# Performance work log

Measured on AMD Instinct MI355X. Metric: run time of the kernel, lower is better.

Reference implementation:

```python
import jax, jax.numpy as jnp
import numpy as np
import math

B, L, LC = 2, 2048, 2048
D_MODEL, D_CROSS, D_HEAD = 1024, 1024, 64
N_HEADS = D_MODEL // D_HEAD
D6 = D_HEAD // 6  # freq bands per spatial axis (k-diffusion AxialRoPE, 3 axes)
EPS = 1e-6


def rope_freqs():
    n = N_HEADS * D6
    f = jnp.exp(jnp.linspace(math.log(math.pi), math.log(10.0 * math.pi), n + 1)[:-1])
    return f.reshape(D6, N_HEADS).T  # [nh, d6]


def rope_theta(pos):
    # pos: [b, l, 3] -> theta: [b, nh, l, 3*d6]
    f = rope_freqs()
    th = jnp.concatenate([pos[..., None, a:a + 1] * f for a in range(3)], axis=-1)  # [b,l,nh,3*d6]
    return jnp.moveaxis(th, -2, -3)


def apply_rotary(x, theta):
    d = theta.shape[-1]
    x1, x2, x3 = x[..., :d], x[..., d:2 * d], x[..., 2 * d:]
    c, s = jnp.cos(theta), jnp.sin(theta)
    return jnp.concatenate([x1 * c - x2 * s, x2 * c + x1 * s, x3], axis=-1)


def rms_norm(x, scale, eps=EPS):
    ms = jnp.mean(x * x, axis=-1, keepdims=True)
    return x * (scale * jax.lax.rsqrt(ms + eps))


def cosine_scale(q, k, scale, eps=EPS):
    s = jnp.sqrt(scale)[:, None, None]  # [nh,1,1]
    qn = q * (s * jax.lax.rsqrt(jnp.sum(q * q, axis=-1, keepdims=True) + eps))
    kn = k * (s * jax.lax.rsqrt(jnp.sum(k * k, axis=-1, keepdims=True) + eps))
    return qn, kn


def setup_inputs():
    key = jax.random.key(0)
    ks = jax.random.split(key, 8)
    return {
        "x": jax.random.normal(ks[0], (B, L, D_MODEL), jnp.float32),
        "pos": jax.random.uniform(ks[1], (B, L, 3), jnp.float32),
        "x_cross": jax.random.normal(ks[2], (B, LC, D_CROSS), jnp.float32),
        "pos_cross": jax.random.uniform(ks[3], (B, LC, 3), jnp.float32),
        "norm_scale": jnp.ones((D_MODEL,), jnp.float32),
        "norm_cross_scale": jnp.ones((D_CROSS,), jnp.float32),
        "q_w": jax.random.normal(ks[4], (D_MODEL, D_MODEL), jnp.float32) * 0.02,
        "kv_w": jax.random.normal(ks[5], (2 * D_MODEL, D_CROSS), jnp.float32) * 0.02,
        "head_scale": jnp.full((N_HEADS,), 10.0, jnp.float32),
        "out_w": jax.random.normal(ks[6], (D_MODEL, D_MODEL), jnp.float32) * 0.02,
    }


def reference(x, pos, x_cross, pos_cross, norm_scale, norm_cross_scale, q_w, kv_w, head_scale, out_w):
    skip = x
    xn = rms_norm(x, norm_scale)
    xc = rms_norm(x_cross, norm_cross_scale)
    q = xn @ q_w.T                       # [b,l,d]
    kv = xc @ kv_w.T                     # [b,lc,2d]
    b, l, _ = q.shape
    lc = kv.shape[1]
    q = q.reshape(b, l, N_HEADS, D_HEAD).transpose(0, 2, 1, 3)          # [b,nh,l,e]
    kv = kv.reshape(b, lc, 2, N_HEADS, D_HEAD)                          # (t nh e) factorization
    k = kv[:, :, 0].transpose(0, 2, 1, 3)
    v = kv[:, :, 1].transpose(0, 2, 1, 3)
    q, k = cosine_scale(q, k, head_scale)
    q = apply_rotary(q, rope_theta(pos))
    k = apply_rotary(k, rope_theta(pos_cross))
    attn = jax.nn.softmax(jnp.einsum('bhqe,bhke->bhqk', q, k), axis=-1)  # scale=1.0 (cosine-sim pre-scaled)
    o = jnp.einsum('bhqk,bhke->bhqe', attn, v)
    o = o.transpose(0, 2, 1, 3).reshape(b, l, D_MODEL)
    return o @ out_w.T + skip
```

## Files before the change

### kernel.cpp

```cpp
#include <hip/hip_runtime.h>

typedef __bf16 bf16_t;
typedef __bf16 bf16x4 __attribute__((ext_vector_type(4)));
typedef __bf16 bf16x8 __attribute__((ext_vector_type(8)));
typedef float f32x4 __attribute__((ext_vector_type(4)));
typedef short s16x4 __attribute__((ext_vector_type(4)));

#define B_DIM 2
#define L_DIM 2048
#define LC_DIM 2048
#define DM 1024
#define NH 16
#define DH 64
#define MB (1u << 20)
#define LOG2E 1.44269504088896f

__device__ __forceinline__ bool probe_is_f32(const unsigned* probe) {
  return probe[0] == 0x3F800000u;
}

__device__ __forceinline__ void async16(const bf16_t* g, bf16_t* l) {
  __builtin_amdgcn_global_load_lds((const __attribute__((address_space(1))) void*)g,
                                   (__attribute__((address_space(3))) void*)l, 16, 0, 0);
}

#if __has_builtin(__builtin_amdgcn_mfma_f32_16x16x16bf16_1k)
#define HAVE_K16 1
__device__ __forceinline__ f32x4 mfma16(bf16x4 a, bf16x4 b, f32x4 c) {
  union { bf16x4 h; s16x4 s; } ua, ub;
  ua.h = a; ub.h = b;
  return __builtin_amdgcn_mfma_f32_16x16x16bf16_1k(ua.s, ub.s, c, 0, 0, 0);
}
#else
#define HAVE_K16 0
#endif

__device__ __forceinline__ void conv_b(const void* src, bf16_t* dst, int i, bool f32) {
  bf16x4 w;
  if (f32) {
    f32x4 v = *(const f32x4*)((const float*)src + i);
    w[0] = (bf16_t)v[0]; w[1] = (bf16_t)v[1]; w[2] = (bf16_t)v[2]; w[3] = (bf16_t)v[3];
  } else {
    w = *(const bf16x4*)((const bf16_t*)src + i);
  }
  *(bf16x4*)(dst + i) = w;
}
__device__ __forceinline__ void conv_f(const void* src, float* dst, int i, int n, bool f32) {
  if (i >= n) return;
  f32x4 v;
  if (f32) {
    v = *(const f32x4*)((const float*)src + i);
  } else {
    bf16x4 w = *(const bf16x4*)((const bf16_t*)src + i);
    v[0] = (float)w[0]; v[1] = (float)w[1]; v[2] = (float)w[2]; v[3] = (float)w[3];
  }
  *(f32x4*)(dst + i) = v;
}

__global__ __launch_bounds__(256) void front_k(
    const void* x, const void* xc, const void* qw, const void* kvw, const void* ow,
    const void* pos, const void* posc, const void* ns, const void* ncs, const void* hs,
    bf16_t* xn, bf16_t* xcn, bf16_t* cqw, bf16_t* ckvw, bf16_t* cow,
    float* fpos, float* fposc, float* fns, float* fncs, float* fhs,
    const unsigned* probe) {
  const bool f32 = probe_is_f32(probe);
  const int tid = threadIdx.x;
  if (blockIdx.x < 2 * B_DIM * L_DIM) {
    const bool isB = blockIdx.x >= B_DIM * L_DIM;
    const int row = isB ? blockIdx.x - B_DIM * L_DIM : blockIdx.x;
    const void* src = isB ? xc : x;
    const void* scr = isB ? ncs : ns;
    bf16_t* out = isB ? xcn : xn;
    float f0, f1, f2, f3, s0, s1, s2, s3;
    if (f32) {
      f32x4 v = *((const f32x4*)((const float*)src + (size_t)row * DM) + tid);
      f0 = v[0]; f1 = v[1]; f2 = v[2]; f3 = v[3];
      f32x4 sv = *((const f32x4*)scr + tid);
      s0 = sv[0]; s1 = sv[1]; s2 = sv[2]; s3 = sv[3];
    } else {
      bf16x4 v = *((const bf16x4*)((const bf16_t*)src + (size_t)row * DM) + tid);
      f0 = (float)v[0]; f1 = (float)v[1]; f2 = (float)v[2]; f3 = (float)v[3];
      bf16x4 sv = *((const bf16x4*)scr + tid);
      s0 = (float)sv[0]; s1 = (float)sv[1]; s2 = (float)sv[2]; s3 = (float)sv[3];
    }
    float ss = f0 * f0 + f1 * f1 + f2 * f2 + f3 * f3;
#pragma unroll
    for (int m = 1; m < 64; m <<= 1) ss += __shfl_xor(ss, m, 64);
    __shared__ float red[4];
    const int wave = tid >> 6, lane = tid & 63;
    if (lane == 0) red[wave] = ss;
    __syncthreads();
    float ms = (red[0] + red[1] + red[2] + red[3]) * (1.0f / DM);
    float r = rsqrtf(ms + 1e-6f);
    bf16x4 w;
    w[0] = (bf16_t)(f0 * r * s0);
    w[1] = (bf16_t)(f1 * r * s1);
    w[2] = (bf16_t)(f2 * r * s2);
    w[3] = (bf16_t)(f3 * r * s3);
    *(bf16x4*)(out + (size_t)row * DM + tid * 4) = w;
    return;
  }
  const int blk = blockIdx.x - 2 * B_DIM * L_DIM;
  const int e4 = tid * 4;
  if (blk < 1024)       conv_b(qw,  cqw,  blk * 1024 + e4, f32);
  else if (blk < 3072)  conv_b(kvw, ckvw, (blk - 1024) * 1024 + e4, f32);
  else if (blk < 4096)  conv_b(ow,  cow,  (blk - 3072) * 1024 + e4, f32);
  else if (blk < 4108)  conv_f(pos,  fpos,  (blk - 4096) * 1024 + e4, 12288, f32);
  else if (blk < 4120)  conv_f(posc, fposc, (blk - 4108) * 1024 + e4, 12288, f32);
  else if (blk == 4120) conv_f(ns,  fns,  e4, 1024, f32);
  else if (blk == 4121) conv_f(ncs, fncs, e4, 1024, f32);
  else                  conv_f(hs,  fhs,  e4, 16, f32);
}

__global__ __launch_bounds__(256) void gemm_qkv_k(const bf16_t* __restrict__ xn,
                                                  const bf16_t* __restrict__ xcn,
                                                  const bf16_t* __restrict__ qw,
                                                  const bf16_t* __restrict__ kvw,
                                                  bf16_t* __restrict__ qb,
                                                  bf16_t* __restrict__ kvK,
                                                  bf16_t* __restrict__ Vp) {
  __shared__ bf16_t Asm[128 * 32];
  __shared__ bf16_t Wsm[128 * 32];
  const int tid = threadIdx.x;
  const int wave = tid >> 6, lane = tid & 63;
  const int quad = lane >> 4, tc = lane & 15;
  const int wr = wave >> 1, wc = wave & 1;
  const bool isq = blockIdx.y < 8;
  const bf16_t* A = isq ? xn : xcn;
  const bf16_t* W = isq ? qw : kvw;
  const int n0 = (isq ? blockIdx.y : (blockIdx.y - 8)) * 128;
  const int m0 = blockIdx.x * 128;
  const int K = 1024;

  const int srow = wave * 16 + (lane >> 2);
  const int scol = (lane & 3) * 8;
  const bf16_t* ag = A + (size_t)(m0 + srow) * K + scol;
  const bf16_t* wg = W + (size_t)(n0 + srow) * K + scol;
  bf16_t* al0 = &Asm[(wave * 16) * 32];
  bf16_t* al1 = &Asm[(64 + wave * 16) * 32];
  bf16_t* wl0 = &Wsm[(wave * 16) * 32];
  bf16_t* wl1 = &Wsm[(64 + wave * 16) * 32];

  f32x4 acc[4][4] = {};

  for (int k0 = 0; k0 < K; k0 += 32) {
    async16(ag + k0, al0);
    async16(ag + k0 + (size_t)64 * K, al1);
    async16(wg + k0, wl0);
    async16(wg + k0 + (size_t)64 * K, wl1);
    __syncthreads();
    bf16x8 af[4], wf[4];
#pragma unroll
    for (int i = 0; i < 4; ++i)
      af[i] = *(const bf16x8*)&Asm[(wr * 64 + i * 16 + tc) * 32 + quad * 8];
#pragma unroll
    for (int j = 0; j < 4; ++j)
      wf[j] = *(const bf16x8*)&Wsm[(wc * 64 + j * 16 + tc) * 32 + quad * 8];
#pragma unroll
    for (int i = 0; i < 4; ++i)
#pragma unroll
      for (int j = 0; j < 4; ++j)
        acc[i][j] = __builtin_amdgcn_mfma_f32_16x16x32_bf16(af[i], wf[j], acc[i][j], 0, 0, 0);
    __syncthreads();
  }

  if (isq || n0 < DM) {
    bf16_t* C = isq ? qb : kvK;
#pragma unroll
    for (int i = 0; i < 4; ++i) {
      const size_t row = (size_t)m0 + wr * 64 + i * 16 + quad * 4;
#pragma unroll
      for (int j = 0; j < 4; ++j) {
        const int col = n0 + wc * 64 + j * 16 + tc;
#pragma unroll
        for (int r = 0; r < 4; ++r)
          C[(row + r) * DM + col] = (bf16_t)acc[i][j][r];
      }
    }
  } else {
#pragma unroll
    for (int i = 0; i < 4; ++i) {
      const int row = m0 + wr * 64 + i * 16 + quad * 4;
      const int b = row >> 11, kc = row & (LC_DIM - 1);
#pragma unroll
      for (int j = 0; j < 4; ++j) {
        const int hd = n0 - DM + wc * 64 + j * 16 + tc;
        const int h = hd >> 6, d = hd & 63;
        bf16x4 pk;
        pk[0] = (bf16_t)acc[i][j][0];
        pk[1] = (bf16_t)acc[i][j][1];
        pk[2] = (bf16_t)acc[i][j][2];
        pk[3] = (bf16_t)acc[i][j][3];
        *(bf16x4*)(Vp + (((size_t)(b * NH + h) * (LC_DIM / 4) + (kc >> 2)) * DH + d) * 4) = pk;
      }
    }
  }
}

__global__ __launch_bounds__(256) void prep_k(bf16_t* __restrict__ q,
                                              const bf16_t* __restrict__ kvK,
                                              bf16_t* __restrict__ Kp,
                                              const float* __restrict__ pos,
                                              const float* __restrict__ pos_cross,
                                              const float* __restrict__ head_scale) {
  const int gw = (blockIdx.x * blockDim.x + threadIdx.x) >> 6;
  const int lane = threadIdx.x & 63;
  const int per = B_DIM * L_DIM * NH;
  const bool is_k = gw >= per;
  const int id = is_k ? gw - per : gw;
  const int h = id & 15;
  const int row = id >> 4;
  const bf16_t* src = (is_k ? kvK : q) + (size_t)row * DM + h * DH;
  const float* pp = (is_k ? pos_cross : pos) + (size_t)row * 3;

  float val = (float)src[lane];
  float ss = val * val;
#pragma unroll
  for (int m = 1; m < 64; m <<= 1) ss += __shfl_xor(ss, m, 64);
  float sc = sqrtf(head_scale[h]) * rsqrtf(ss + 1e-6f);
  if (!is_k) sc *= LOG2E;
  float vn = val * sc;

  const int j = lane;
  const int tj = j < 30 ? j : (j < 60 ? j - 30 : 0);
  const int a = tj >= 20 ? 2 : (tj >= 10 ? 1 : 0);
  const int jj = tj - a * 10;
  float p = pp[a];
  float freq = 3.14159265358979f * expf((float)(jj * 16 + h) * 0.014391156831f);
  float th = p * freq;
  float cth = cosf(th), sth = sinf(th);
  const int partner = j < 30 ? j + 30 : (j < 60 ? j - 30 : j);
  float vp = __shfl(vn, partner, 64);
  float outv;
  if (j < 30)       outv = vn * cth - vp * sth;
  else if (j < 60)  outv = vn * cth + vp * sth;
  else              outv = vn;

  if (is_k) {
    const int b = row >> 11, l = row & (LC_DIM - 1);
    Kp[(((size_t)b * NH + h) * LC_DIM + l) * DH + lane] = (bf16_t)outv;
  } else {
    q[(size_t)row * DM + h * DH + lane] = (bf16_t)outv;
  }
}

#define FLASH_LOAD(KB, VB, KC)                                                   \
  {                                                                              \
    _Pragma("unroll") for (int mt = 0; mt < 4; ++mt) {                           \
      _Pragma("unroll") for (int hf = 0; hf < 2; ++hf)                           \
        KB[mt][hf] = *(const bf16x8*)(kg + (size_t)((KC) + mt * 16 + tc) * DH +  \
                                      hf * 32 + quad * 8);                       \
      _Pragma("unroll") for (int dt = 0; dt < 4; ++dt)                           \
        VB[mt][dt] = *(const bf16x4*)(vp + ((size_t)(((KC) >> 2) + mt * 4 + quad) * DH + \
                                            dt * 16 + tc) * 4);                  \
    }                                                                            \
  }

#define FLASH_COMPUTE(KB, VB)                                                    \
  {                                                                              \
    _Pragma("unroll") for (int jj = 0; jj < 4; ++jj) {                           \
      f32x4 s[4];                                                                \
      _Pragma("unroll") for (int mt = 0; mt < 4; ++mt) {                         \
        f32x4 zf = {0.f, 0.f, 0.f, 0.f};                                         \
        zf = __builtin_amdgcn_mfma_f32_16x16x32_bf16(KB[mt][0], qf[jj][0], zf, 0, 0, 0); \
        zf = __builtin_amdgcn_mfma_f32_16x16x32_bf16(KB[mt][1], qf[jj][1], zf, 0, 0, 0); \
        s[mt] = zf;                                                              \
      }                                                                          \
      bf16x4 p[4];                                                               \
      _Pragma("unroll") for (int mt = 0; mt < 4; ++mt) {                         \
        p[mt][0] = (bf16_t)__builtin_amdgcn_exp2f(s[mt][0]);                     \
        p[mt][1] = (bf16_t)__builtin_amdgcn_exp2f(s[mt][1]);                     \
        p[mt][2] = (bf16_t)__builtin_amdgcn_exp2f(s[mt][2]);                     \
        p[mt][3] = (bf16_t)__builtin_amdgcn_exp2f(s[mt][3]);                     \
      }                                                                          \
      _Pragma("unroll") for (int mt = 0; mt < 4; ++mt) {                         \
        accL[jj] = mfma16(p[mt], ones, accL[jj]);                                \
        _Pragma("unroll") for (int dt = 0; dt < 4; ++dt)                         \
          accO[jj][dt] = mfma16(p[mt], VB[mt][dt], accO[jj][dt]);                \
      }                                                                          \
    }                                                                            \
  }

__global__ __launch_bounds__(64, 2) void flash7_k(const bf16_t* __restrict__ q,
                                                  const bf16_t* __restrict__ Kp,
                                                  const bf16_t* __restrict__ Vp,
                                                  bf16_t* __restrict__ Op,
                                                  float* __restrict__ lp) {
  const int lane = threadIdx.x;
  const int quad = lane >> 4, tc = lane & 15;
  const int bh = blockIdx.y, b = bh >> 4;
  const int z = blockIdx.z;
  const int q0 = blockIdx.x * 64;

  bf16x8 qf[4][2];
#pragma unroll
  for (int jj = 0; jj < 4; ++jj)
#pragma unroll
    for (int hf = 0; hf < 2; ++hf)
      qf[jj][hf] = *(const bf16x8*)(q + (size_t)(b * L_DIM + q0 + jj * 16 + tc) * DM +
                                    (bh & 15) * DH + hf * 32 + quad * 8);

  f32x4 accO[4][4] = {};
  const bf16_t* kg = Kp + (size_t)bh * LC_DIM * DH;
  const bf16_t* vp = Vp + (size_t)bh * (LC_DIM / 4) * DH * 4;
  const int base = z * 1024;

#if HAVE_K16
  f32x4 accL[4] = {};
  bf16x4 ones;
  ones[0] = (bf16_t)1.0f; ones[1] = (bf16_t)1.0f;
  ones[2] = (bf16_t)1.0f; ones[3] = (bf16_t)1.0f;

  bf16x8 k0f[4][2], k1f[4][2];
  bf16x4 v0f[4][4], v1f[4][4];
  FLASH_LOAD(k0f, v0f, base);
#pragma unroll 1
  for (int kc0 = base; kc0 < base + 1024; kc0 += 128) {
    FLASH_LOAD(k1f, v1f, kc0 + 64);
    FLASH_COMPUTE(k0f, v0f);
    if (kc0 + 128 < base + 1024) FLASH_LOAD(k0f, v0f, kc0 + 128);
    FLASH_COMPUTE(k1f, v1f);
  }
#else
  __shared__ bf16_t Psm[64 * 64];
  float lsum[4] = {0.f, 0.f, 0.f, 0.f};
  const int sw = tc & 7;
#pragma unroll 1
  for (int kc0 = base; kc0 < base + 1024; kc0 += 64) {
    bf16x8 kfr[4][2];
#pragma unroll
    for (int mt = 0; mt < 4; ++mt)
#pragma unroll
      for (int hf = 0; hf < 2; ++hf)
        kfr[mt][hf] = *(const bf16x8*)(kg + (size_t)(kc0 + mt * 16 + tc) * DH +
                                       hf * 32 + quad * 8);
#pragma unroll
    for (int jj = 0; jj < 4; ++jj) {
      f32x4 s[4];
#pragma unroll
      for (int mt = 0; mt < 4; ++mt) {
        f32x4 zf = {0.f, 0.f, 0.f, 0.f};
        zf = __builtin_amdgcn_mfma_f32_16x16x32_bf16(kfr[mt][0], qf[jj][0], zf, 0, 0, 0);
        zf = __builtin_amdgcn_mfma_f32_16x16x32_bf16(kfr[mt][1], qf[jj][1], zf, 0, 0, 0);
        s[mt] = zf;
      }
#pragma unroll
      for (int mt = 0; mt < 4; ++mt) {
        float p0 = __builtin_amdgcn_exp2f(s[mt][0]);
        float p1 = __builtin_amdgcn_exp2f(s[mt][1]);
        float p2 = __builtin_amdgcn_exp2f(s[mt][2]);
        float p3 = __builtin_amdgcn_exp2f(s[mt][3]);
        lsum[jj] += (p0 + p1) + (p2 + p3);
        bf16x4 pk;
        pk[0] = (bf16_t)p0; pk[1] = (bf16_t)p1; pk[2] = (bf16_t)p2; pk[3] = (bf16_t)p3;
        const int phys = (mt * 2 + (quad >> 1)) ^ sw;
        *(bf16x4*)&Psm[(jj * 16 + tc) * 64 + phys * 8 + (quad & 1) * 4] = pk;
      }
    }
#pragma unroll
    for (int kb = 0; kb < 2; ++kb) {
      bf16x8 vfull[4];
#pragma unroll
      for (int dt = 0; dt < 4; ++dt) {
        const size_t k4 = (size_t)((kc0 + kb * 32) >> 2) + quad * 2;
        bf16x4 lo = *(const bf16x4*)(vp + (k4 * DH + dt * 16 + tc) * 4);
        bf16x4 hi = *(const bf16x4*)(vp + ((k4 + 1) * DH + dt * 16 + tc) * 4);
#pragma unroll
        for (int e = 0; e < 4; ++e) { vfull[dt][e] = lo[e]; vfull[dt][4 + e] = hi[e]; }
      }
#pragma unroll
      for (int jp = 0; jp < 4; ++jp) {
        bf16x8 pf = *(const bf16x8*)&Psm[(jp * 16 + tc) * 64 + ((kb * 4 + quad) ^ sw) * 8];
#pragma unroll
        for (int dt = 0; dt < 4; ++dt)
          accO[jp][dt] = __builtin_amdgcn_mfma_f32_16x16x32_bf16(pf, vfull[dt], accO[jp][dt], 0, 0, 0);
      }
    }
  }
#endif

  bf16_t* Ob = Op + (size_t)(z * 32 + bh) * L_DIM * DH;
  float* lb = lp + (size_t)(z * 32 + bh) * L_DIM;
#if HAVE_K16
#pragma unroll
  for (int jj = 0; jj < 4; ++jj) {
    if (tc == 0) {
#pragma unroll
      for (int r = 0; r < 4; ++r) lb[q0 + jj * 16 + quad * 4 + r] = accL[jj][r];
    }
#pragma unroll
    for (int r = 0; r < 4; ++r) {
      const size_t qg = q0 + jj * 16 + quad * 4 + r;
#pragma unroll
      for (int dt = 0; dt < 4; ++dt)
        Ob[qg * DH + dt * 16 + tc] = (bf16_t)accO[jj][dt][r];
    }
  }
#else
#pragma unroll
  for (int jj = 0; jj < 4; ++jj) {
    lsum[jj] += __shfl_xor(lsum[jj], 16, 64);
    lsum[jj] += __shfl_xor(lsum[jj], 32, 64);
  }
#pragma unroll
  for (int jj = 0; jj < 4; ++jj) {
    if (quad == 0) lb[q0 + jj * 16 + tc] = lsum[jj];
#pragma unroll
    for (int r = 0; r < 4; ++r) {
      const size_t qg = q0 + jj * 16 + quad * 4 + r;
#pragma unroll
      for (int dt = 0; dt < 4; ++dt)
        Ob[qg * DH + dt * 16 + tc] = (bf16_t)accO[jj][dt][r];
    }
  }
#endif
}

__global__ __launch_bounds__(256) void combine_k(const bf16_t* __restrict__ Op,
                                                 const float* __restrict__ lp,
                                                 bf16_t* __restrict__ ob) {
  const size_t t = (size_t)blockIdx.x * 256 + threadIdx.x;
  const int bh = (int)(t >> 15);
  const int rem = (int)(t & 32767);
  const int l = rem >> 4, d4 = (rem & 15) * 4;
  const size_t base = ((size_t)bh * L_DIM + l) * DH + d4;
  const size_t zoff = (size_t)32 * L_DIM * DH;
  bf16x4 a0 = *(const bf16x4*)(Op + base);
  bf16x4 a1 = *(const bf16x4*)(Op + zoff + base);
  const float linv = 1.f / (lp[(size_t)bh * L_DIM + l] + lp[(size_t)32 * L_DIM + bh * L_DIM + l]);
  bf16x4 w;
#pragma unroll
  for (int e = 0; e < 4; ++e) w[e] = (bf16_t)(((float)a0[e] + (float)a1[e]) * linv);
  const int b = bh >> 4, h = bh & 15;
  *(bf16x4*)(ob + ((size_t)(b * L_DIM + l)) * DM + h * DH + d4) = w;
}

__global__ __launch_bounds__(256) void gemm_out_k(const bf16_t* __restrict__ A,
                                                  const bf16_t* __restrict__ W,
                                                  const void* __restrict__ skip_raw,
                                                  void* __restrict__ out,
                                                  const unsigned* __restrict__ probe) {
  __shared__ bf16_t Asm[64 * 32];
  __shared__ bf16_t Wsm[128 * 32];
  const int tid = threadIdx.x;
  const int wave = tid >> 6, lane = tid & 63;
  const int quad = lane >> 4, tc = lane & 15;
  const int wr = wave >> 1, wc = wave & 1;
  const int m0 = blockIdx.x * 64, n0 = blockIdx.y * 128;
  const int K = 1024, N = 1024;

  const int srow = wave * 16 + (lane >> 2);
  const int scol = (lane & 3) * 8;
  const bf16_t* ag = A + (size_t)(m0 + srow) * K + scol;
  const bf16_t* wg = W + (size_t)(n0 + srow) * K + scol;
  bf16_t* al = &Asm[(wave * 16) * 32];
  bf16_t* wl0 = &Wsm[(wave * 16) * 32];
  bf16_t* wl1 = &Wsm[(64 + wave * 16) * 32];

  f32x4 acc[2][4] = {};

  for (int k0 = 0; k0 < K; k0 += 32) {
    async16(ag + k0, al);
    async16(wg + k0, wl0);
    async16(wg + k0 + (size_t)64 * K, wl1);
    __syncthreads();
    bf16x8 af[2], wf[4];
#pragma unroll
    for (int i = 0; i < 2; ++i)
      af[i] = *(const bf16x8*)&Asm[(wr * 32 + i * 16 + tc) * 32 + quad * 8];
#pragma unroll
    for (int j = 0; j < 4; ++j)
      wf[j] = *(const bf16x8*)&Wsm[(wc * 64 + j * 16 + tc) * 32 + quad * 8];
#pragma unroll
    for (int i = 0; i < 2; ++i)
#pragma unroll
      for (int j = 0; j < 4; ++j)
        acc[i][j] = __builtin_amdgcn_mfma_f32_16x16x32_bf16(af[i], wf[j], acc[i][j], 0, 0, 0);
    __syncthreads();
  }

  const bool f32o = probe_is_f32(probe);
#pragma unroll
  for (int i = 0; i < 2; ++i) {
    const size_t row = (size_t)m0 + wr * 32 + i * 16 + quad * 4;
#pragma unroll
    for (int j = 0; j < 4; ++j) {
      const int col = n0 + wc * 64 + j * 16 + tc;
#pragma unroll
      for (int r = 0; r < 4; ++r) {
        const size_t idx = (row + r) * (size_t)N + col;
        float v = acc[i][j][r];
        if (f32o) {
          v += ((const float*)skip_raw)[idx];
          ((float*)out)[idx] = v;
        } else {
          v += (float)((const bf16_t*)skip_raw)[idx];
          ((bf16_t*)out)[idx] = (bf16_t)v;
        }
      }
    }
  }
}

extern "C" void kernel_launch(void* const* d_in, const int* in_sizes, int n_in,
                              void* d_out, int out_size, void* d_ws, size_t ws_size,
                              hipStream_t stream) {
  const unsigned* probe = (const unsigned*)d_in[4];
  char* ws = (char*)d_ws;

  bf16_t* cow  = (bf16_t*)(ws + 0 * MB);
  bf16_t* cqw  = (bf16_t*)(ws + 2 * MB);
  bf16_t* ckvw = (bf16_t*)(ws + 4 * MB);
  bf16_t* xn   = (bf16_t*)(ws + 8 * MB);
  bf16_t* xcn  = (bf16_t*)(ws + 16 * MB);
  bf16_t* Op   = (bf16_t*)(ws + 8 * MB);
  bf16_t* kvK  = (bf16_t*)(ws + 24 * MB);
  bf16_t* qb   = (bf16_t*)(ws + 32 * MB);
  bf16_t* Vp   = (bf16_t*)(ws + 40 * MB);
  bf16_t* Kp   = (bf16_t*)(ws + 48 * MB);
  bf16_t* ob   = (bf16_t*)(ws + 56 * MB);
  float* lp    = (float*)(ws + 64 * MB);
  float* fpos  = (float*)(ws + 65 * MB);
  float* fposc = (float*)(ws + 65 * MB + 64 * 1024);
  float* fns   = (float*)(ws + 65 * MB + 128 * 1024);
  float* fncs  = (float*)(ws + 65 * MB + 144 * 1024);
  float* fhs   = (float*)(ws + 65 * MB + 160 * 1024);

  front_k<<<2 * B_DIM * L_DIM + 4123, 256, 0, stream>>>(
      d_in[0], d_in[2], d_in[6], d_in[7], d_in[9], d_in[1], d_in[3], d_in[4],
      d_in[5], d_in[8], xn, xcn, cqw, ckvw, cow, fpos, fposc, fns, fncs, fhs, probe);
  gemm_qkv_k<<<dim3(32, 24), 256, 0, stream>>>(xn, xcn, cqw, ckvw, qb, kvK, Vp);
  prep_k<<<(2 * B_DIM * L_DIM * NH) / 4, 256, 0, stream>>>(qb, kvK, Kp, fpos, fposc, fhs);
  flash7_k<<<dim3(L_DIM / 64, B_DIM * NH, 2), 64, 0, stream>>>(qb, Kp, Vp, Op, lp);
  combine_k<<<4096, 256, 0, stream>>>(Op, lp, ob);
  gemm_out_k<<<dim3(64, 8), 256, 0, stream>>>(ob, cow, d_in[0], d_out, probe);
}
```

Baseline: 267.5 us.

## Fuse split-K attention combine into flash kernel via intra-block LDS reduction

The attention kernel now uses 4 waves per block, each handling a quarter of the key range for the same 64 queries. The partial outputs and row sums are reduced through shared memory in a tree, then normalized and written straight to the head-interleaved output. This removes the separate combine kernel, the partial-output and row-sum round trip through global memory, and a launch. In exchange it adds block-level barriers and about 40KB of LDS per block, which may limit occupancy, and waves idle during the reduction.

```diff
diff --git a/kernel.cpp b/kernel.cpp
--- a/kernel.cpp
+++ b/kernel.cpp
@@ -281,15 +281,32 @@
     }                                                                            \
   }
 
-__global__ __launch_bounds__(64, 2) void flash7_k(const bf16_t* __restrict__ q,
-                                                  const bf16_t* __restrict__ Kp,
-                                                  const bf16_t* __restrict__ Vp,
-                                                  bf16_t* __restrict__ Op,
-                                                  float* __restrict__ lp) {
-  const int lane = threadIdx.x;
+#define CB_PUBLISH(BP)                                                           \
+  {                                                                              \
+    _Pragma("unroll") for (int jj = 0; jj < 4; ++jj) {                           \
+      _Pragma("unroll") for (int dt = 0; dt < 4; ++dt)                           \
+        *(f32x4*)&(BP)[((jj * 4 + dt) * 64 + lane) * 4] = accO[jj][dt];          \
+      *(f32x4*)&(BP)[((16 + jj) * 64 + lane) * 4] = accL[jj];                    \
+    }                                                                            \
+  }
+#define CB_ACCUM(BP)                                                             \
+  {                                                                              \
+    _Pragma("unroll") for (int jj = 0; jj < 4; ++jj) {                           \
+      _Pragma("unroll") for (int dt = 0; dt < 4; ++dt)                           \
+        accO[jj][dt] += *(const f32x4*)&(BP)[((jj * 4 + dt) * 64 + lane) * 4];   \
+      accL[jj] += *(const f32x4*)&(BP)[((16 + jj) * 64 + lane) * 4];             \
+    }                                                                            \
+  }
+
+__global__ __launch_bounds__(256, 4) void flash8_k(const bf16_t* __restrict__ q,
+                                                   const bf16_t* __restrict__ Kp,
+                                                   const bf16_t* __restrict__ Vp,
+                                                   bf16_t* __restrict__ ob) {
+  const int tid = threadIdx.x;
+  const int wave = tid >> 6;
+  const int lane = tid & 63;
   const int quad = lane >> 4, tc = lane & 15;
-  const int bh = blockIdx.y, b = bh >> 4;
-  const int z = blockIdx.z;
+  const int bh = blockIdx.y, b = bh >> 4, h = bh & 15;
   const int q0 = blockIdx.x * 64;
 
   bf16x8 qf[4][2];
@@ -298,15 +315,15 @@
 #pragma unroll
     for (int hf = 0; hf < 2; ++hf)
       qf[jj][hf] = *(const bf16x8*)(q + (size_t)(b * L_DIM + q0 + jj * 16 + tc) * DM +
-                                    (bh & 15) * DH + hf * 32 + quad * 8);
+                                    h * DH + hf * 32 + quad * 8);
 
   f32x4 accO[4][4] = {};
+  f32x4 accL[4] = {};
   const bf16_t* kg = Kp + (size_t)bh * LC_DIM * DH;
   const bf16_t* vp = Vp + (size_t)bh * (LC_DIM / 4) * DH * 4;
-  const int base = z * 1024;
+  const int base = wave * 512;
 
 #if HAVE_K16
-  f32x4 accL[4] = {};
   bf16x4 ones;
   ones[0] = (bf16_t)1.0f; ones[1] = (bf16_t)1.0f;
   ones[2] = (bf16_t)1.0f; ones[3] = (bf16_t)1.0f;
@@ -315,10 +332,10 @@
   bf16x4 v0f[4][4], v1f[4][4];
   FLASH_LOAD(k0f, v0f, base);
 #pragma unroll 1
-  for (int kc0 = base; kc0 < base + 1024; kc0 += 128) {
+  for (int kc0 = base; kc0 < base + 512; kc0 += 128) {
     FLASH_LOAD(k1f, v1f, kc0 + 64);
     FLASH_COMPUTE(k0f, v0f);
-    if (kc0 + 128 < base + 1024) FLASH_LOAD(k0f, v0f, kc0 + 128);
+    if (kc0 + 128 < base + 512) FLASH_LOAD(k0f, v0f, kc0 + 128);
     FLASH_COMPUTE(k1f, v1f);
   }
 #else
@@ -326,7 +343,7 @@
   float lsum[4] = {0.f, 0.f, 0.f, 0.f};
   const int sw = tc & 7;
 #pragma unroll 1
-  for (int kc0 = base; kc0 < base + 1024; kc0 += 64) {
+  for (int kc0 = base; kc0 < base + 512; kc0 += 64) {
     bf16x8 kfr[4][2];
 #pragma unroll
     for (int mt = 0; mt < 4; ++mt)
@@ -377,62 +394,39 @@
       }
     }
   }
-#endif
-
-  bf16_t* Ob = Op + (size_t)(z * 32 + bh) * L_DIM * DH;
-  float* lb = lp + (size_t)(z * 32 + bh) * L_DIM;
-#if HAVE_K16
-#pragma unroll
-  for (int jj = 0; jj < 4; ++jj) {
-    if (tc == 0) {
-#pragma unroll
-      for (int r = 0; r < 4; ++r) lb[q0 + jj * 16 + quad * 4 + r] = accL[jj][r];
-    }
-#pragma unroll
-    for (int r = 0; r < 4; ++r) {
-      const size_t qg = q0 + jj * 16 + quad * 4 + r;
-#pragma unroll
-      for (int dt = 0; dt < 4; ++dt)
-        Ob[qg * DH + dt * 16 + tc] = (bf16_t)accO[jj][dt][r];
-    }
-  }
-#else
 #pragma unroll
   for (int jj = 0; jj < 4; ++jj) {
     lsum[jj] += __shfl_xor(lsum[jj], 16, 64);
     lsum[jj] += __shfl_xor(lsum[jj], 32, 64);
-  }
-#pragma unroll
-  for (int jj = 0; jj < 4; ++jj) {
-    if (quad == 0) lb[q0 + jj * 16 + tc] = lsum[jj];
-#pragma unroll
-    for (int r = 0; r < 4; ++r) {
-      const size_t qg = q0 + jj * 16 + quad * 4 + r;
-#pragma unroll
-      for (int dt = 0; dt < 4; ++dt)
-        Ob[qg * DH + dt * 16 + tc] = (bf16_t)accO[jj][dt][r];
-    }
+#pragma unroll
+    for (int r = 0; r < 4; ++r) accL[jj][r] = __shfl(lsum[jj], quad * 4 + r, 64);
   }
 #endif
-}
-
-__global__ __launch_bounds__(256) void combine_k(const bf16_t* __restrict__ Op,
-                                                 const float* __restrict__ lp,
-                                                 bf16_t* __restrict__ ob) {
-  const size_t t = (size_t)blockIdx.x * 256 + threadIdx.x;
-  const int bh = (int)(t >> 15);
-  const int rem = (int)(t & 32767);
-  const int l = rem >> 4, d4 = (rem & 15) * 4;
-  const size_t base = ((size_t)bh * L_DIM + l) * DH + d4;
-  const size_t zoff = (size_t)32 * L_DIM * DH;
-  bf16x4 a0 = *(const bf16x4*)(Op + base);
-  bf16x4 a1 = *(const bf16x4*)(Op + zoff + base);
-  const float linv = 1.f / (lp[(size_t)bh * L_DIM + l] + lp[(size_t)32 * L_DIM + bh * L_DIM + l]);
-  bf16x4 w;
-#pragma unroll
-  for (int e = 0; e < 4; ++e) w[e] = (bf16_t)(((float)a0[e] + (float)a1[e]) * linv);
-  const int b = bh >> 4, h = bh & 15;
-  *(bf16x4*)(ob + ((size_t)(b * L_DIM + l)) * DM + h * DH + d4) = w;
+
+  __shared__ float cbuf[2][64 * 80];
+  if (wave & 1) CB_PUBLISH(cbuf[wave >> 1]);
+  __syncthreads();
+  if (!(wave & 1)) CB_ACCUM(cbuf[wave >> 1]);
+  __syncthreads();
+  if (wave == 2) CB_PUBLISH(cbuf[0]);
+  __syncthreads();
+  if (wave == 0) {
+    CB_ACCUM(cbuf[0]);
+    bf16_t* og = ob + ((size_t)(b * L_DIM + q0)) * DM + h * DH;
+#pragma unroll
+    for (int jj = 0; jj < 4; ++jj) {
+      f32x4 linv;
+#pragma unroll
+      for (int r = 0; r < 4; ++r) linv[r] = 1.0f / accL[jj][r];
+#pragma unroll
+      for (int r = 0; r < 4; ++r) {
+        const size_t row = (size_t)(jj * 16 + quad * 4 + r) * DM;
+#pragma unroll
+        for (int dt = 0; dt < 4; ++dt)
+          og[row + dt * 16 + tc] = (bf16_t)(accO[jj][dt][r] * linv[r]);
+      }
+    }
+  }
 }
 
 __global__ __launch_bounds__(256) void gemm_out_k(const bf16_t* __restrict__ A,
@@ -513,13 +507,11 @@
   bf16_t* ckvw = (bf16_t*)(ws + 4 * MB);
   bf16_t* xn   = (bf16_t*)(ws + 8 * MB);
   bf16_t* xcn  = (bf16_t*)(ws + 16 * MB);
-  bf16_t* Op   = (bf16_t*)(ws + 8 * MB);
   bf16_t* kvK  = (bf16_t*)(ws + 24 * MB);
   bf16_t* qb   = (bf16_t*)(ws + 32 * MB);
   bf16_t* Vp   = (bf16_t*)(ws + 40 * MB);
   bf16_t* Kp   = (bf16_t*)(ws + 48 * MB);
   bf16_t* ob   = (bf16_t*)(ws + 56 * MB);
-  float* lp    = (float*)(ws + 64 * MB);
   float* fpos  = (float*)(ws + 65 * MB);
   float* fposc = (float*)(ws + 65 * MB + 64 * 1024);
   float* fns   = (float*)(ws + 65 * MB + 128 * 1024);
@@ -531,7 +523,6 @@
       d_in[5], d_in[8], xn, xcn, cqw, ckvw, cow, fpos, fposc, fns, fncs, fhs, probe);
   gemm_qkv_k<<<dim3(32, 24), 256, 0, stream>>>(xn, xcn, cqw, ckvw, qb, kvK, Vp);
   prep_k<<<(2 * B_DIM * L_DIM * NH) / 4, 256, 0, stream>>>(qb, kvK, Kp, fpos, fposc, fhs);
-  flash7_k<<<dim3(L_DIM / 64, B_DIM * NH, 2), 64, 0, stream>>>(qb, Kp, Vp, Op, lp);
-  combine_k<<<4096, 256, 0, stream>>>(Op, lp, ob);
+  flash8_k<<<dim3(L_DIM / 64, B_DIM * NH), 256, 0, stream>>>(qb, Kp, Vp, ob);
   gemm_out_k<<<dim3(64, 8), 256, 0, stream>>>(ob, cow, d_in[0], d_out, probe);
 }
```

New measurement: 685.9 us. 156% more time.

## Fuse split-K combine into output GEMM and compute row sums on VALU

Applied to the files above, without the earlier changes.

Removes the separate combine kernel by having the output GEMM read both split-K partial outputs and row sums directly, normalising them while staging the A tile into LDS. Inside the flash loop, the row-sum MFMA against a ones vector is replaced by scalar float accumulation of the exponentials with a cross-lane shuffle at the end. The compute phase is also bracketed with s_setprio to favour MFMA issue. The trade-off is that A loading in the GEMM becomes synchronous global loads plus VALU work, replacing the async LDS loads, and the intermediate ob buffer round trip is dropped.

```diff
diff --git a/kernel.cpp b/kernel.cpp
--- a/kernel.cpp
+++ b/kernel.cpp
@@ -14,6 +14,8 @@
 #define DH 64
 #define MB (1u << 20)
 #define LOG2E 1.44269504088896f
+#define NZ 2
+#define SPAN (LC_DIM / NZ)
 
 __device__ __forceinline__ bool probe_is_f32(const unsigned* probe) {
   return probe[0] == 0x3F800000u;
@@ -258,6 +260,7 @@
 
 #define FLASH_COMPUTE(KB, VB)                                                    \
   {                                                                              \
+    __builtin_amdgcn_s_setprio(1);                                               \
     _Pragma("unroll") for (int jj = 0; jj < 4; ++jj) {                           \
       f32x4 s[4];                                                                \
       _Pragma("unroll") for (int mt = 0; mt < 4; ++mt) {                         \
@@ -268,24 +271,27 @@
       }                                                                          \
       bf16x4 p[4];                                                               \
       _Pragma("unroll") for (int mt = 0; mt < 4; ++mt) {                         \
-        p[mt][0] = (bf16_t)__builtin_amdgcn_exp2f(s[mt][0]);                     \
-        p[mt][1] = (bf16_t)__builtin_amdgcn_exp2f(s[mt][1]);                     \
-        p[mt][2] = (bf16_t)__builtin_amdgcn_exp2f(s[mt][2]);                     \
-        p[mt][3] = (bf16_t)__builtin_amdgcn_exp2f(s[mt][3]);                     \
+        float e0 = __builtin_amdgcn_exp2f(s[mt][0]);                             \
+        float e1 = __builtin_amdgcn_exp2f(s[mt][1]);                             \
+        float e2 = __builtin_amdgcn_exp2f(s[mt][2]);                             \
+        float e3 = __builtin_amdgcn_exp2f(s[mt][3]);                             \
+        lsum[jj] += (e0 + e1) + (e2 + e3);                                       \
+        p[mt][0] = (bf16_t)e0; p[mt][1] = (bf16_t)e1;                            \
+        p[mt][2] = (bf16_t)e2; p[mt][3] = (bf16_t)e3;                            \
       }                                                                          \
       _Pragma("unroll") for (int mt = 0; mt < 4; ++mt) {                         \
-        accL[jj] = mfma16(p[mt], ones, accL[jj]);                                \
         _Pragma("unroll") for (int dt = 0; dt < 4; ++dt)                         \
           accO[jj][dt] = mfma16(p[mt], VB[mt][dt], accO[jj][dt]);                \
       }                                                                          \
     }                                                                            \
-  }
-
-__global__ __launch_bounds__(64, 2) void flash7_k(const bf16_t* __restrict__ q,
-                                                  const bf16_t* __restrict__ Kp,
-                                                  const bf16_t* __restrict__ Vp,
-                                                  bf16_t* __restrict__ Op,
-                                                  float* __restrict__ lp) {
+    __builtin_amdgcn_s_setprio(0);                                               \
+  }
+
+__global__ __launch_bounds__(64, 2) void flash11_k(const bf16_t* __restrict__ q,
+                                                   const bf16_t* __restrict__ Kp,
+                                                   const bf16_t* __restrict__ Vp,
+                                                   bf16_t* __restrict__ Op,
+                                                   float* __restrict__ lp) {
   const int lane = threadIdx.x;
   const int quad = lane >> 4, tc = lane & 15;
   const int bh = blockIdx.y, b = bh >> 4;
@@ -301,32 +307,27 @@
                                     (bh & 15) * DH + hf * 32 + quad * 8);
 
   f32x4 accO[4][4] = {};
+  float lsum[4] = {0.f, 0.f, 0.f, 0.f};
   const bf16_t* kg = Kp + (size_t)bh * LC_DIM * DH;
   const bf16_t* vp = Vp + (size_t)bh * (LC_DIM / 4) * DH * 4;
-  const int base = z * 1024;
+  const int base = z * SPAN;
 
 #if HAVE_K16
-  f32x4 accL[4] = {};
-  bf16x4 ones;
-  ones[0] = (bf16_t)1.0f; ones[1] = (bf16_t)1.0f;
-  ones[2] = (bf16_t)1.0f; ones[3] = (bf16_t)1.0f;
-
   bf16x8 k0f[4][2], k1f[4][2];
   bf16x4 v0f[4][4], v1f[4][4];
   FLASH_LOAD(k0f, v0f, base);
 #pragma unroll 1
-  for (int kc0 = base; kc0 < base + 1024; kc0 += 128) {
+  for (int kc0 = base; kc0 < base + SPAN; kc0 += 128) {
     FLASH_LOAD(k1f, v1f, kc0 + 64);
     FLASH_COMPUTE(k0f, v0f);
-    if (kc0 + 128 < base + 1024) FLASH_LOAD(k0f, v0f, kc0 + 128);
+    if (kc0 + 128 < base + SPAN) FLASH_LOAD(k0f, v0f, kc0 + 128);
     FLASH_COMPUTE(k1f, v1f);
   }
 #else
   __shared__ bf16_t Psm[64 * 64];
-  float lsum[4] = {0.f, 0.f, 0.f, 0.f};
   const int sw = tc & 7;
 #pragma unroll 1
-  for (int kc0 = base; kc0 < base + 1024; kc0 += 64) {
+  for (int kc0 = base; kc0 < base + SPAN; kc0 += 64) {
     bf16x8 kfr[4][2];
 #pragma unroll
     for (int mt = 0; mt < 4; ++mt)
@@ -381,22 +382,6 @@
 
   bf16_t* Ob = Op + (size_t)(z * 32 + bh) * L_DIM * DH;
   float* lb = lp + (size_t)(z * 32 + bh) * L_DIM;
-#if HAVE_K16
-#pragma unroll
-  for (int jj = 0; jj < 4; ++jj) {
-    if (tc == 0) {
-#pragma unroll
-      for (int r = 0; r < 4; ++r) lb[q0 + jj * 16 + quad * 4 + r] = accL[jj][r];
-    }
-#pragma unroll
-    for (int r = 0; r < 4; ++r) {
-      const size_t qg = q0 + jj * 16 + quad * 4 + r;
-#pragma unroll
-      for (int dt = 0; dt < 4; ++dt)
-        Ob[qg * DH + dt * 16 + tc] = (bf16_t)accO[jj][dt][r];
-    }
-  }
-#else
 #pragma unroll
   for (int jj = 0; jj < 4; ++jj) {
     lsum[jj] += __shfl_xor(lsum[jj], 16, 64);
@@ -413,29 +398,10 @@
         Ob[qg * DH + dt * 16 + tc] = (bf16_t)accO[jj][dt][r];
     }
   }
-#endif
-}
-
-__global__ __launch_bounds__(256) void combine_k(const bf16_t* __restrict__ Op,
-                                                 const float* __restrict__ lp,
-                                                 bf16_t* __restrict__ ob) {
-  const size_t t = (size_t)blockIdx.x * 256 + threadIdx.x;
-  const int bh = (int)(t >> 15);
-  const int rem = (int)(t & 32767);
-  const int l = rem >> 4, d4 = (rem & 15) * 4;
-  const size_t base = ((size_t)bh * L_DIM + l) * DH + d4;
-  const size_t zoff = (size_t)32 * L_DIM * DH;
-  bf16x4 a0 = *(const bf16x4*)(Op + base);
-  bf16x4 a1 = *(const bf16x4*)(Op + zoff + base);
-  const float linv = 1.f / (lp[(size_t)bh * L_DIM + l] + lp[(size_t)32 * L_DIM + bh * L_DIM + l]);
-  bf16x4 w;
-#pragma unroll
-  for (int e = 0; e < 4; ++e) w[e] = (bf16_t)(((float)a0[e] + (float)a1[e]) * linv);
-  const int b = bh >> 4, h = bh & 15;
-  *(bf16x4*)(ob + ((size_t)(b * L_DIM + l)) * DM + h * DH + d4) = w;
-}
-
-__global__ __launch_bounds__(256) void gemm_out_k(const bf16_t* __restrict__ A,
+}
+
+__global__ __launch_bounds__(256) void gemm_out_k(const bf16_t* __restrict__ Op,
+                                                  const float* __restrict__ lp,
                                                   const bf16_t* __restrict__ W,
                                                   const void* __restrict__ skip_raw,
                                                   void* __restrict__ out,
@@ -451,18 +417,30 @@
 
   const int srow = wave * 16 + (lane >> 2);
   const int scol = (lane & 3) * 8;
-  const bf16_t* ag = A + (size_t)(m0 + srow) * K + scol;
+  const int arow = m0 + srow;
+  const int bb = arow >> 11, l = arow & (L_DIM - 1);
+  const size_t zoff = (size_t)32 * L_DIM * DH;
   const bf16_t* wg = W + (size_t)(n0 + srow) * K + scol;
-  bf16_t* al = &Asm[(wave * 16) * 32];
   bf16_t* wl0 = &Wsm[(wave * 16) * 32];
   bf16_t* wl1 = &Wsm[(64 + wave * 16) * 32];
 
   f32x4 acc[2][4] = {};
+  float linv = 0.f;
 
   for (int k0 = 0; k0 < K; k0 += 32) {
-    async16(ag + k0, al);
     async16(wg + k0, wl0);
     async16(wg + k0 + (size_t)64 * K, wl1);
+    const int bh = bb * NH + (k0 >> 6);
+    if ((k0 & 63) == 0)
+      linv = 1.f / (lp[(size_t)bh * L_DIM + l] + lp[(size_t)(32 + bh) * L_DIM + l]);
+    const size_t obase = ((size_t)bh * L_DIM + l) * DH + (k0 & 63) + scol;
+    bf16x8 a0 = *(const bf16x8*)(Op + obase);
+    bf16x8 a1 = *(const bf16x8*)(Op + zoff + obase);
+    bf16x8 aw;
+#pragma unroll
+    for (int e = 0; e < 8; ++e)
+      aw[e] = (bf16_t)(((float)a0[e] + (float)a1[e]) * linv);
+    *(bf16x8*)&Asm[srow * 32 + scol] = aw;
     __syncthreads();
     bf16x8 af[2], wf[4];
 #pragma unroll
@@ -518,7 +496,6 @@
   bf16_t* qb   = (bf16_t*)(ws + 32 * MB);
   bf16_t* Vp   = (bf16_t*)(ws + 40 * MB);
   bf16_t* Kp   = (bf16_t*)(ws + 48 * MB);
-  bf16_t* ob   = (bf16_t*)(ws + 56 * MB);
   float* lp    = (float*)(ws + 64 * MB);
   float* fpos  = (float*)(ws + 65 * MB);
   float* fposc = (float*)(ws + 65 * MB + 64 * 1024);
@@ -531,7 +508,6 @@
       d_in[5], d_in[8], xn, xcn, cqw, ckvw, cow, fpos, fposc, fns, fncs, fhs, probe);
   gemm_qkv_k<<<dim3(32, 24), 256, 0, stream>>>(xn, xcn, cqw, ckvw, qb, kvK, Vp);
   prep_k<<<(2 * B_DIM * L_DIM * NH) / 4, 256, 0, stream>>>(qb, kvK, Kp, fpos, fposc, fhs);
-  flash7_k<<<dim3(L_DIM / 64, B_DIM * NH, 2), 64, 0, stream>>>(qb, Kp, Vp, Op, lp);
-  combine_k<<<4096, 256, 0, stream>>>(Op, lp, ob);
-  gemm_out_k<<<dim3(64, 8), 256, 0, stream>>>(ob, cow, d_in[0], d_out, probe);
-}
+  flash11_k<<<dim3(L_DIM / 64, B_DIM * NH, NZ), 64, 0, stream>>>(qb, Kp, Vp, Op, lp);
+  gemm_out_k<<<dim3(64, 8), 256, 0, stream>>>(Op, lp, cow, d_in[0], d_out, probe);
+}
```

Measured after the change: 386.0 us. 44.3% more time.
